# Kernel tuning notes

Hardware: AMD Instinct MI355X
Metric: run time of the kernel (lower is better)

## Reference

```python
import jax, jax.numpy as jnp
import numpy as np

N = 50000          # nodes
E = 1_600_000      # edges (avg degree 32)
D = 128            # input_dim
H = 128            # hidden_dim
EPS = 1e-5


def setup_inputs() -> dict:
    key = jax.random.key(0)
    ks = jax.random.split(key, 8)
    x = jax.random.normal(ks[0], (N, D), jnp.float32)
    edge_index = jax.random.randint(ks[1], (2, E), 0, N)
    message = jax.random.normal(ks[2], (E, H), jnp.float32)

    def lin(k, fin, fout):
        return jax.random.normal(k, (fin, fout), jnp.float32) / np.sqrt(fin).astype(np.float32)

    return {
        "x": x,
        "message": message,
        "W1": lin(ks[3], D + 2 * H, H), "b1": jnp.zeros((H,), jnp.float32),
        "g1": jnp.ones((H,), jnp.float32), "be1": jnp.zeros((H,), jnp.float32),
        "W2": lin(ks[4], H, H), "b2": jnp.zeros((H,), jnp.float32),
        "g2": jnp.ones((H,), jnp.float32), "be2": jnp.zeros((H,), jnp.float32),
        "Wa": lin(ks[5], H, 1), "ba": jnp.zeros((1,), jnp.float32),
        "edge_index": edge_index,
    }


def _batchnorm(h, g, b):
    # training-mode BatchNorm1d: biased batch stats over the node dim
    mu = h.mean(axis=0)
    var = h.var(axis=0)
    return (h - mu) * jax.lax.rsqrt(var + EPS) * g + b


def reference(x, message, W1, b1, g1, be1, W2, b2, g2, be2, Wa, ba, edge_index):
    row, col = edge_index[0], edge_index[1]
    n = x.shape[0]

    def smax(idx):
        m = jax.ops.segment_max(message, idx, num_segments=n)  # [N, H]
        # torch_scatter scatter(reduce='max') leaves empty slots at 0
        return jnp.where(jnp.isfinite(m), m, jnp.zeros_like(m))

    fwd = smax(col)
    bwd = smax(row)
    out = jnp.concatenate([x, fwd, bwd], axis=1)  # [N, D+2H]

    h = jax.nn.relu(_batchnorm(out @ W1 + b1, g1, be1))  # dropout = identity (eval)
    h = jax.nn.relu(_batchnorm(h @ W2 + b2, g2, be2))
    att = jax.nn.sigmoid(h @ Wa + ba).reshape(-1)        # [N]
    return h, att
```

## Files before the change

kernel.cpp:

```cpp
#include <hip/hip_runtime.h>
#include <math.h>

#define N_NODES 50000
#define N_EDGES 1600000
#define DIM 128
#define EPS 1e-5f
#define CAP 96

typedef short bf16x8 __attribute__((ext_vector_type(8)));
typedef float f32x4 __attribute__((ext_vector_type(4)));
typedef int i32x4 __attribute__((ext_vector_type(4)));
typedef unsigned short ushort_t;

__device__ __forceinline__ f32x4 v4max(f32x4 a, f32x4 b) {
    f32x4 r;
    r[0] = fmaxf(a[0], b[0]); r[1] = fmaxf(a[1], b[1]);
    r[2] = fmaxf(a[2], b[2]); r[3] = fmaxf(a[3], b[3]);
    return r;
}

__device__ __forceinline__ ushort_t f2bf(float f) {
    unsigned int u = __float_as_uint(f);
    return (ushort_t)((u + 0x7FFFu + ((u >> 16) & 1u)) >> 16);
}
__device__ __forceinline__ float bf2f(ushort_t u) {
    return __uint_as_float(((unsigned int)u) << 16);
}

__global__ __launch_bounds__(256) void k_prep(const float* __restrict__ W1, const float* __restrict__ W2,
                                              ushort_t* __restrict__ W1t, ushort_t* __restrict__ W2t) {
    int gid = blockIdx.x * 256 + threadIdx.x;
    if (gid < 128 * 384) {
        int j = gid / 384, k = gid % 384;
        W1t[gid] = f2bf(W1[k * 128 + j]);
    } else {
        int g2 = gid - 128 * 384;
        if (g2 < 128 * 128) {
            int j = g2 / 128, k = g2 % 128;
            W2t[g2] = f2bf(W2[k * 128 + j]);
        }
    }
}

__global__ __launch_bounds__(256) void k_bucket(const int* __restrict__ ei, int* __restrict__ cnt,
                                                int* __restrict__ slots) {
    int t = blockIdx.x * 256 + threadIdx.x;
    if (t >= N_EDGES / 4) return;
    int4 r4 = reinterpret_cast<const int4*>(ei)[t];
    int4 c4 = reinterpret_cast<const int4*>(ei + N_EDGES)[t];
    int e = t * 4;
    slots[c4.x * CAP + atomicAdd(&cnt[c4.x], 1)] = e + 0;
    slots[c4.y * CAP + atomicAdd(&cnt[c4.y], 1)] = e + 1;
    slots[c4.z * CAP + atomicAdd(&cnt[c4.z], 1)] = e + 2;
    slots[c4.w * CAP + atomicAdd(&cnt[c4.w], 1)] = e + 3;
    slots[(N_NODES + r4.x) * CAP + atomicAdd(&cnt[N_NODES + r4.x], 1)] = e + 0;
    slots[(N_NODES + r4.y) * CAP + atomicAdd(&cnt[N_NODES + r4.y], 1)] = e + 1;
    slots[(N_NODES + r4.z) * CAP + atomicAdd(&cnt[N_NODES + r4.z], 1)] = e + 2;
    slots[(N_NODES + r4.w) * CAP + atomicAdd(&cnt[N_NODES + r4.w], 1)] = e + 3;
}

__global__ __launch_bounds__(256) void k_gather(const f32x4* __restrict__ msgv,
                                                const int* __restrict__ slots,
                                                const int* __restrict__ cnt,
                                                ushort_t* __restrict__ fwd,
                                                ushort_t* __restrict__ bwd) {
    const int wid = blockIdx.x * 4 + (threadIdx.x >> 6);
    const int dir = (wid >= N_NODES);
    const int n = dir ? wid - N_NODES : wid;
    const int lane = threadIdx.x & 63;
    const int q = lane & 31;
    const int h = lane >> 5;
    const int c = cnt[dir * N_NODES + n];
    const int* el = slots + (size_t)(dir * N_NODES + n) * CAP;

    f32x4 acc0 = {-INFINITY, -INFINITY, -INFINITY, -INFINITY};
    f32x4 acc1 = acc0;
    const int nfull = c >> 2;
    int g = h;
    for (; g + 2 < nfull; g += 4) {
        i32x4 ea = *reinterpret_cast<const i32x4*>(el + g * 4);
        i32x4 eb = *reinterpret_cast<const i32x4*>(el + (g + 2) * 4);
        f32x4 m0 = __builtin_nontemporal_load(&msgv[(size_t)ea[0] * 32 + q]);
        f32x4 m1 = __builtin_nontemporal_load(&msgv[(size_t)ea[1] * 32 + q]);
        f32x4 m2 = __builtin_nontemporal_load(&msgv[(size_t)ea[2] * 32 + q]);
        f32x4 m3 = __builtin_nontemporal_load(&msgv[(size_t)ea[3] * 32 + q]);
        f32x4 m4 = __builtin_nontemporal_load(&msgv[(size_t)eb[0] * 32 + q]);
        f32x4 m5 = __builtin_nontemporal_load(&msgv[(size_t)eb[1] * 32 + q]);
        f32x4 m6 = __builtin_nontemporal_load(&msgv[(size_t)eb[2] * 32 + q]);
        f32x4 m7 = __builtin_nontemporal_load(&msgv[(size_t)eb[3] * 32 + q]);
        acc0 = v4max(acc0, v4max(v4max(m0, m1), v4max(m2, m3)));
        acc1 = v4max(acc1, v4max(v4max(m4, m5), v4max(m6, m7)));
    }
    for (; g < nfull; g += 2) {
        i32x4 e4 = *reinterpret_cast<const i32x4*>(el + g * 4);
        f32x4 m0 = __builtin_nontemporal_load(&msgv[(size_t)e4[0] * 32 + q]);
        f32x4 m1 = __builtin_nontemporal_load(&msgv[(size_t)e4[1] * 32 + q]);
        f32x4 m2 = __builtin_nontemporal_load(&msgv[(size_t)e4[2] * 32 + q]);
        f32x4 m3 = __builtin_nontemporal_load(&msgv[(size_t)e4[3] * 32 + q]);
        acc0 = v4max(acc0, v4max(v4max(m0, m1), v4max(m2, m3)));
    }
    if (h == (nfull & 1)) {
        for (int p = nfull * 4; p < c; ++p) {
            acc1 = v4max(acc1, __builtin_nontemporal_load(&msgv[(size_t)el[p] * 32 + q]));
        }
    }
    f32x4 acc = v4max(acc0, acc1);
    acc[0] = fmaxf(acc[0], __shfl_xor(acc[0], 32));
    acc[1] = fmaxf(acc[1], __shfl_xor(acc[1], 32));
    acc[2] = fmaxf(acc[2], __shfl_xor(acc[2], 32));
    acc[3] = fmaxf(acc[3], __shfl_xor(acc[3], 32));

    if (h == 0) {
        if (c == 0) { acc[0] = 0.f; acc[1] = 0.f; acc[2] = 0.f; acc[3] = 0.f; }
        ushort_t pk[4] = {f2bf(acc[0]), f2bf(acc[1]), f2bf(acc[2]), f2bf(acc[3])};
        ushort_t* dst = (dir ? bwd : fwd) + n * DIM + q * 4;
        *reinterpret_cast<uint2*>(dst) = *reinterpret_cast<const uint2*>(pk);
    }
}


__global__ __launch_bounds__(256) void k_gemm1(const float* __restrict__ x,
                                               const ushort_t* __restrict__ fwd,
                                               const ushort_t* __restrict__ bwd,
                                               const ushort_t* __restrict__ W1t,
                                               const float* __restrict__ b1,
                                               ushort_t* __restrict__ h1b,
                                               float* __restrict__ stats) {
    __shared__ uint4 rowsA4[512];
    __shared__ uint4 Wt4[1024];
    __shared__ float bias[128];
    __shared__ float s_sum[128], s_sq[128];
    char* rowsA = (char*)rowsA4;
    char* Wt = (char*)Wt4;

    const int tid = threadIdx.x;
    const int wid = tid >> 6;
    const int lane = tid & 63;
    const int ln15 = lane & 15;
    const int kb16 = (lane >> 4) * 16;
    const int n0 = blockIdx.x * 64;
    const int rA = wid * 16 + ln15;
    const int rsw = (rA & 7) << 4;

    if (tid < 128) { bias[tid] = b1[tid]; s_sum[tid] = 0.0f; s_sq[tid] = 0.0f; }

    f32x4 acc[8];
#pragma unroll
    for (int i = 0; i < 8; ++i) acc[i] = (f32x4){0.0f, 0.0f, 0.0f, 0.0f};

    for (int c = 0; c < 6; ++c) {
        const int koff = (c & 1) * 64;
        __syncthreads();
        if (c < 2) {
#pragma unroll
            for (int i = 0; i < 2; ++i) {
                int g = tid + i * 256;
                int r = g >> 3, k8 = g & 7;
                int n = n0 + r;
                f32x4 v0 = {0.f, 0.f, 0.f, 0.f}, v1 = v0;
                if (n < N_NODES) {
                    const f32x4* p = reinterpret_cast<const f32x4*>(x + n * DIM + koff + k8 * 8);
                    v0 = __builtin_nontemporal_load(p);
                    v1 = __builtin_nontemporal_load(p + 1);
                }
                ushort_t pk[8] = {f2bf(v0[0]), f2bf(v0[1]), f2bf(v0[2]), f2bf(v0[3]),
                                  f2bf(v1[0]), f2bf(v1[1]), f2bf(v1[2]), f2bf(v1[3])};
                *(uint4*)(rowsA + ((r * 128 + k8 * 16) ^ ((r & 7) << 4))) = *(const uint4*)pk;
            }
        } else {
            const ushort_t* src16 = (c < 4) ? fwd : bwd;
#pragma unroll
            for (int i = 0; i < 2; ++i) {
                int g = tid + i * 256;
                int r = g >> 3, k8 = g & 7;
                int n = n0 + r;
                uint4 v = make_uint4(0u, 0u, 0u, 0u);
                if (n < N_NODES) v = *reinterpret_cast<const uint4*>(src16 + n * DIM + koff + k8 * 8);
                *(uint4*)(rowsA + ((r * 128 + k8 * 16) ^ ((r & 7) << 4))) = v;
            }
        }
#pragma unroll
        for (int i = 0; i < 4; ++i) {
            int g = tid + i * 256;
            int j = g >> 3, k8 = g & 7;
            uint4 w = *reinterpret_cast<const uint4*>(W1t + j * 384 + c * 64 + k8 * 8);
            *(uint4*)(Wt + ((j * 128 + k8 * 16) ^ ((j & 7) << 4))) = w;
        }
        __syncthreads();
#pragma unroll
        for (int ks = 0; ks < 2; ++ks) {
            bf16x8 a = *(bf16x8*)(rowsA + ((rA * 128 + ks * 64 + kb16) ^ rsw));
#pragma unroll
            for (int ct = 0; ct < 8; ++ct) {
                int j = ct * 16 + ln15;
                bf16x8 b = *(bf16x8*)(Wt + ((j * 128 + ks * 64 + kb16) ^ ((j & 7) << 4)));
                acc[ct] = __builtin_amdgcn_mfma_f32_16x16x32_bf16(a, b, acc[ct], 0, 0, 0);
            }
        }
    }
    __syncthreads();
    const int jcol = ln15;
#pragma unroll
    for (int ct = 0; ct < 8; ++ct) {
        int j = ct * 16 + jcol;
        float bj = bias[j];
        float s = 0.0f, q = 0.0f;
#pragma unroll
        for (int r = 0; r < 4; ++r) {
            int n = n0 + wid * 16 + (lane >> 4) * 4 + r;
            if (n < N_NODES) {
                float v = acc[ct][r] + bj;
                h1b[n * DIM + j] = f2bf(v);
                s += v; q += v * v;
            }
        }
        s += __shfl_xor(s, 16); s += __shfl_xor(s, 32);
        q += __shfl_xor(q, 16); q += __shfl_xor(q, 32);
        if ((lane >> 4) == 0) { atomicAdd(&s_sum[j], s); atomicAdd(&s_sq[j], q); }
    }
    __syncthreads();
    if (tid < 128) {
        atomicAdd(&stats[tid], s_sum[tid]);
        atomicAdd(&stats[128 + tid], s_sq[tid]);
    }
}

__global__ __launch_bounds__(256) void k_gemm2(const ushort_t* __restrict__ h1b,
                                               const ushort_t* __restrict__ W2t,
                                               const float* __restrict__ b2,
                                               const float* __restrict__ g1,
                                               const float* __restrict__ be1,
                                               ushort_t* __restrict__ h2b,
                                               float* __restrict__ stats) {
    __shared__ uint4 rowsA4[512];
    __shared__ uint4 Wt4[1024];
    __shared__ float bias[128];
    __shared__ float ssc[128], ssh[128];
    __shared__ float s_sum[128], s_sq[128];
    char* rowsA = (char*)rowsA4;
    char* Wt = (char*)Wt4;

    const int tid = threadIdx.x;
    const int wid = tid >> 6;
    const int lane = tid & 63;
    const int ln15 = lane & 15;
    const int kb16 = (lane >> 4) * 16;
    const int n0 = blockIdx.x * 64;
    const int rA = wid * 16 + ln15;
    const int rsw = (rA & 7) << 4;

    if (tid < 128) {
        float mu = stats[tid] * (1.0f / N_NODES);
        float var = stats[128 + tid] * (1.0f / N_NODES) - mu * mu;
        float sc = rsqrtf(var + EPS) * g1[tid];
        ssc[tid] = sc;
        ssh[tid] = be1[tid] - mu * sc;
        bias[tid] = b2[tid];
        s_sum[tid] = 0.0f; s_sq[tid] = 0.0f;
    }

    f32x4 acc[8];
#pragma unroll
    for (int i = 0; i < 8; ++i) acc[i] = (f32x4){0.0f, 0.0f, 0.0f, 0.0f};

    for (int c = 0; c < 2; ++c) {
        const int koff = c * 64;
        __syncthreads();
#pragma unroll
        for (int i = 0; i < 2; ++i) {
            int g = tid + i * 256;
            int r = g >> 3, k8 = g & 7;
            int n = n0 + r;
            ushort_t pk[8] = {0, 0, 0, 0, 0, 0, 0, 0};
            if (n < N_NODES) {
                uint4 raw = *reinterpret_cast<const uint4*>(h1b + n * DIM + koff + k8 * 8);
                const ushort_t* rp = (const ushort_t*)&raw;
#pragma unroll
                for (int t = 0; t < 8; ++t) {
                    int kk = koff + k8 * 8 + t;
                    float v = fmaxf(bf2f(rp[t]) * ssc[kk] + ssh[kk], 0.0f);
                    pk[t] = f2bf(v);
                }
            }
            *(uint4*)(rowsA + ((r * 128 + k8 * 16) ^ ((r & 7) << 4))) = *(const uint4*)pk;
        }
#pragma unroll
        for (int i = 0; i < 4; ++i) {
            int g = tid + i * 256;
            int j = g >> 3, k8 = g & 7;
            uint4 w = *reinterpret_cast<const uint4*>(W2t + j * 128 + c * 64 + k8 * 8);
            *(uint4*)(Wt + ((j * 128 + k8 * 16) ^ ((j & 7) << 4))) = w;
        }
        __syncthreads();
#pragma unroll
        for (int ks = 0; ks < 2; ++ks) {
            bf16x8 a = *(bf16x8*)(rowsA + ((rA * 128 + ks * 64 + kb16) ^ rsw));
#pragma unroll
            for (int ct = 0; ct < 8; ++ct) {
                int j = ct * 16 + ln15;
                bf16x8 b = *(bf16x8*)(Wt + ((j * 128 + ks * 64 + kb16) ^ ((j & 7) << 4)));
                acc[ct] = __builtin_amdgcn_mfma_f32_16x16x32_bf16(a, b, acc[ct], 0, 0, 0);
            }
        }
    }
    __syncthreads();
    const int jcol = ln15;
#pragma unroll
    for (int ct = 0; ct < 8; ++ct) {
        int j = ct * 16 + jcol;
        float bj = bias[j];
        float s = 0.0f, q = 0.0f;
#pragma unroll
        for (int r = 0; r < 4; ++r) {
            int n = n0 + wid * 16 + (lane >> 4) * 4 + r;
            if (n < N_NODES) {
                float v = acc[ct][r] + bj;
                h2b[n * DIM + j] = f2bf(v);
                s += v; q += v * v;
            }
        }
        s += __shfl_xor(s, 16); s += __shfl_xor(s, 32);
        q += __shfl_xor(q, 16); q += __shfl_xor(q, 32);
        if ((lane >> 4) == 0) { atomicAdd(&s_sum[j], s); atomicAdd(&s_sq[j], q); }
    }
    __syncthreads();
    if (tid < 128) {
        atomicAdd(&stats[256 + tid], s_sum[tid]);
        atomicAdd(&stats[384 + tid], s_sq[tid]);
    }
}

__global__ __launch_bounds__(256) void k_final(const ushort_t* __restrict__ h2b,
                                               const float* __restrict__ stats,
                                               const float* __restrict__ g2,
                                               const float* __restrict__ be2,
                                               const float* __restrict__ Wa,
                                               const float* __restrict__ ba,
                                               float* __restrict__ out) {
    const int lane = threadIdx.x & 63;
    const int wv = threadIdx.x >> 6;
    const int n = blockIdx.x * 4 + wv;
    if (n >= N_NODES) return;
    const int j0 = lane, j1 = lane + 64;

    float mu0 = stats[256 + j0] * (1.0f / N_NODES);
    float var0 = stats[384 + j0] * (1.0f / N_NODES) - mu0 * mu0;
    float sc0 = rsqrtf(var0 + EPS) * g2[j0];
    float sh0 = be2[j0] - mu0 * sc0;
    float mu1 = stats[256 + j1] * (1.0f / N_NODES);
    float var1 = stats[384 + j1] * (1.0f / N_NODES) - mu1 * mu1;
    float sc1 = rsqrtf(var1 + EPS) * g2[j1];
    float sh1 = be2[j1] - mu1 * sc1;

    float v0 = fmaxf(bf2f(h2b[n * DIM + j0]) * sc0 + sh0, 0.0f);
    float v1 = fmaxf(bf2f(h2b[n * DIM + j1]) * sc1 + sh1, 0.0f);
    out[n * DIM + j0] = v0;
    out[n * DIM + j1] = v1;

    float p = v0 * Wa[j0] + v1 * Wa[j1];
#pragma unroll
    for (int off = 32; off > 0; off >>= 1) p += __shfl_down(p, off);
    if (lane == 0) out[N_NODES * DIM + n] = 1.0f / (1.0f + expf(-(p + ba[0])));
}

extern "C" void kernel_launch(void* const* d_in, const int* in_sizes, int n_in,
                              void* d_out, int out_size, void* d_ws, size_t ws_size,
                              hipStream_t stream) {
    const float* x   = (const float*)d_in[0];
    const float* msg = (const float*)d_in[1];
    const float* W1  = (const float*)d_in[2];
    const float* b1  = (const float*)d_in[3];
    const float* g1  = (const float*)d_in[4];
    const float* be1 = (const float*)d_in[5];
    const float* W2  = (const float*)d_in[6];
    const float* b2  = (const float*)d_in[7];
    const float* g2  = (const float*)d_in[8];
    const float* be2 = (const float*)d_in[9];
    const float* Wa  = (const float*)d_in[10];
    const float* ba  = (const float*)d_in[11];
    const int*   ei  = (const int*)d_in[12];

    float*    stats = (float*)d_ws;
    ushort_t* fwdb  = (ushort_t*)(stats + 512);
    ushort_t* bwdb  = fwdb + N_NODES * DIM;
    int*      cnt   = (int*)(bwdb + N_NODES * DIM);
    int*      slots = cnt + 2 * N_NODES;
    ushort_t* W1t   = (ushort_t*)(slots + 2 * N_NODES * CAP);
    ushort_t* W2t   = W1t + 128 * 384;

    ushort_t* h1b = (ushort_t*)d_out;
    ushort_t* h2b = fwdb;
    float*    out = (float*)d_out;

    (void)hipMemsetAsync(stats, 0, 512 * sizeof(float), stream);
    (void)hipMemsetAsync(cnt, 0, 2 * N_NODES * sizeof(int), stream);
    k_prep<<<(128 * 384 + 128 * 128 + 255) / 256, 256, 0, stream>>>(W1, W2, W1t, W2t);
    k_bucket<<<(N_EDGES / 4 + 255) / 256, 256, 0, stream>>>(ei, cnt, slots);
    k_gather<<<(2 * N_NODES) / 4, 256, 0, stream>>>((const f32x4*)msg, slots, cnt, fwdb, bwdb);
    k_gemm1<<<(N_NODES + 63) / 64, 256, 0, stream>>>(x, fwdb, bwdb, W1t, b1, h1b, stats);
    k_gemm2<<<(N_NODES + 63) / 64, 256, 0, stream>>>(h1b, W2t, b2, g1, be1, h2b, stats);
    k_final<<<(N_NODES + 3) / 4, 256, 0, stream>>>(h2b, stats, g2, be2, Wa, ba, out);
}
```

Measured before the change: 621.2 us.

## Pre-convert messages to bf16 in bucketing kernel and gather bf16 rows

New measurement: 690.0 us. 11.1% more time.

```diff
diff --git a/kernel.cpp b/kernel.cpp
--- a/kernel.cpp
+++ b/kernel.cpp
@@ -10,21 +10,20 @@
 typedef short bf16x8 __attribute__((ext_vector_type(8)));
 typedef float f32x4 __attribute__((ext_vector_type(4)));
 typedef int i32x4 __attribute__((ext_vector_type(4)));
+typedef unsigned int u32x2 __attribute__((ext_vector_type(2)));
 typedef unsigned short ushort_t;
 
-__device__ __forceinline__ f32x4 v4max(f32x4 a, f32x4 b) {
-    f32x4 r;
-    r[0] = fmaxf(a[0], b[0]); r[1] = fmaxf(a[1], b[1]);
-    r[2] = fmaxf(a[2], b[2]); r[3] = fmaxf(a[3], b[3]);
-    return r;
-}
-
-__device__ __forceinline__ ushort_t f2bf(float f) {
+__device__ __forceinline__ unsigned int f2bf(float f) {
     unsigned int u = __float_as_uint(f);
-    return (ushort_t)((u + 0x7FFFu + ((u >> 16) & 1u)) >> 16);
+    return (u + 0x7FFFu + ((u >> 16) & 1u)) >> 16;
 }
 __device__ __forceinline__ float bf2f(ushort_t u) {
     return __uint_as_float(((unsigned int)u) << 16);
+}
+
+__device__ __forceinline__ void wmax(unsigned int w, float& lo, float& hi) {
+    lo = fmaxf(lo, __uint_as_float(w << 16));
+    hi = fmaxf(hi, __uint_as_float(w & 0xFFFF0000u));
 }
 
 __global__ __launch_bounds__(256) void k_prep(const float* __restrict__ W1, const float* __restrict__ W2,
@@ -32,34 +31,46 @@
     int gid = blockIdx.x * 256 + threadIdx.x;
     if (gid < 128 * 384) {
         int j = gid / 384, k = gid % 384;
-        W1t[gid] = f2bf(W1[k * 128 + j]);
+        W1t[gid] = (ushort_t)f2bf(W1[k * 128 + j]);
     } else {
         int g2 = gid - 128 * 384;
         if (g2 < 128 * 128) {
             int j = g2 / 128, k = g2 % 128;
-            W2t[g2] = f2bf(W2[k * 128 + j]);
-        }
-    }
-}
-
-__global__ __launch_bounds__(256) void k_bucket(const int* __restrict__ ei, int* __restrict__ cnt,
-                                                int* __restrict__ slots) {
+            W2t[g2] = (ushort_t)f2bf(W2[k * 128 + j]);
+        }
+    }
+}
+
+__global__ __launch_bounds__(256) void k_bucketconv(const int* __restrict__ ei, int* __restrict__ cnt,
+                                                    int* __restrict__ slots,
+                                                    const f32x4* __restrict__ msg,
+                                                    u32x2* __restrict__ msgb) {
     int t = blockIdx.x * 256 + threadIdx.x;
-    if (t >= N_EDGES / 4) return;
-    int4 r4 = reinterpret_cast<const int4*>(ei)[t];
-    int4 c4 = reinterpret_cast<const int4*>(ei + N_EDGES)[t];
-    int e = t * 4;
-    slots[c4.x * CAP + atomicAdd(&cnt[c4.x], 1)] = e + 0;
-    slots[c4.y * CAP + atomicAdd(&cnt[c4.y], 1)] = e + 1;
-    slots[c4.z * CAP + atomicAdd(&cnt[c4.z], 1)] = e + 2;
-    slots[c4.w * CAP + atomicAdd(&cnt[c4.w], 1)] = e + 3;
-    slots[(N_NODES + r4.x) * CAP + atomicAdd(&cnt[N_NODES + r4.x], 1)] = e + 0;
-    slots[(N_NODES + r4.y) * CAP + atomicAdd(&cnt[N_NODES + r4.y], 1)] = e + 1;
-    slots[(N_NODES + r4.z) * CAP + atomicAdd(&cnt[N_NODES + r4.z], 1)] = e + 2;
-    slots[(N_NODES + r4.w) * CAP + atomicAdd(&cnt[N_NODES + r4.w], 1)] = e + 3;
-}
-
-__global__ __launch_bounds__(256) void k_gather(const f32x4* __restrict__ msgv,
+    if (t < N_EDGES / 4) {
+        int4 r4 = reinterpret_cast<const int4*>(ei)[t];
+        int4 c4 = reinterpret_cast<const int4*>(ei + N_EDGES)[t];
+        int e = t * 4;
+        slots[c4.x * CAP + atomicAdd(&cnt[c4.x], 1)] = e + 0;
+        slots[c4.y * CAP + atomicAdd(&cnt[c4.y], 1)] = e + 1;
+        slots[c4.z * CAP + atomicAdd(&cnt[c4.z], 1)] = e + 2;
+        slots[c4.w * CAP + atomicAdd(&cnt[c4.w], 1)] = e + 3;
+        slots[(N_NODES + r4.x) * CAP + atomicAdd(&cnt[N_NODES + r4.x], 1)] = e + 0;
+        slots[(N_NODES + r4.y) * CAP + atomicAdd(&cnt[N_NODES + r4.y], 1)] = e + 1;
+        slots[(N_NODES + r4.z) * CAP + atomicAdd(&cnt[N_NODES + r4.z], 1)] = e + 2;
+        slots[(N_NODES + r4.w) * CAP + atomicAdd(&cnt[N_NODES + r4.w], 1)] = e + 3;
+    }
+    const size_t total = (size_t)N_EDGES * 32;
+    const size_t stride = (size_t)gridDim.x * 256;
+    for (size_t v = t; v < total; v += stride) {
+        f32x4 m = __builtin_nontemporal_load(&msg[v]);
+        u32x2 o;
+        o[0] = f2bf(m[0]) | (f2bf(m[1]) << 16);
+        o[1] = f2bf(m[2]) | (f2bf(m[3]) << 16);
+        msgb[v] = o;
+    }
+}
+
+__global__ __launch_bounds__(256) void k_gather(const u32x2* __restrict__ msgb,
                                                 const int* __restrict__ slots,
                                                 const int* __restrict__ cnt,
                                                 ushort_t* __restrict__ fwd,
@@ -73,48 +84,62 @@
     const int c = cnt[dir * N_NODES + n];
     const int* el = slots + (size_t)(dir * N_NODES + n) * CAP;
 
-    f32x4 acc0 = {-INFINITY, -INFINITY, -INFINITY, -INFINITY};
-    f32x4 acc1 = acc0;
+    float l0a = -INFINITY, h0a = -INFINITY, l1a = -INFINITY, h1a = -INFINITY;
+    float l0b = -INFINITY, h0b = -INFINITY, l1b = -INFINITY, h1b = -INFINITY;
     const int nfull = c >> 2;
     int g = h;
     for (; g + 2 < nfull; g += 4) {
         i32x4 ea = *reinterpret_cast<const i32x4*>(el + g * 4);
         i32x4 eb = *reinterpret_cast<const i32x4*>(el + (g + 2) * 4);
-        f32x4 m0 = __builtin_nontemporal_load(&msgv[(size_t)ea[0] * 32 + q]);
-        f32x4 m1 = __builtin_nontemporal_load(&msgv[(size_t)ea[1] * 32 + q]);
-        f32x4 m2 = __builtin_nontemporal_load(&msgv[(size_t)ea[2] * 32 + q]);
-        f32x4 m3 = __builtin_nontemporal_load(&msgv[(size_t)ea[3] * 32 + q]);
-        f32x4 m4 = __builtin_nontemporal_load(&msgv[(size_t)eb[0] * 32 + q]);
-        f32x4 m5 = __builtin_nontemporal_load(&msgv[(size_t)eb[1] * 32 + q]);
-        f32x4 m6 = __builtin_nontemporal_load(&msgv[(size_t)eb[2] * 32 + q]);
-        f32x4 m7 = __builtin_nontemporal_load(&msgv[(size_t)eb[3] * 32 + q]);
-        acc0 = v4max(acc0, v4max(v4max(m0, m1), v4max(m2, m3)));
-        acc1 = v4max(acc1, v4max(v4max(m4, m5), v4max(m6, m7)));
+        u32x2 m0 = msgb[(size_t)ea[0] * 32 + q];
+        u32x2 m1 = msgb[(size_t)ea[1] * 32 + q];
+        u32x2 m2 = msgb[(size_t)ea[2] * 32 + q];
+        u32x2 m3 = msgb[(size_t)ea[3] * 32 + q];
+        u32x2 m4 = msgb[(size_t)eb[0] * 32 + q];
+        u32x2 m5 = msgb[(size_t)eb[1] * 32 + q];
+        u32x2 m6 = msgb[(size_t)eb[2] * 32 + q];
+        u32x2 m7 = msgb[(size_t)eb[3] * 32 + q];
+        wmax(m0[0], l0a, h0a); wmax(m0[1], l1a, h1a);
+        wmax(m1[0], l0a, h0a); wmax(m1[1], l1a, h1a);
+        wmax(m2[0], l0a, h0a); wmax(m2[1], l1a, h1a);
+        wmax(m3[0], l0a, h0a); wmax(m3[1], l1a, h1a);
+        wmax(m4[0], l0b, h0b); wmax(m4[1], l1b, h1b);
+        wmax(m5[0], l0b, h0b); wmax(m5[1], l1b, h1b);
+        wmax(m6[0], l0b, h0b); wmax(m6[1], l1b, h1b);
+        wmax(m7[0], l0b, h0b); wmax(m7[1], l1b, h1b);
     }
     for (; g < nfull; g += 2) {
         i32x4 e4 = *reinterpret_cast<const i32x4*>(el + g * 4);
-        f32x4 m0 = __builtin_nontemporal_load(&msgv[(size_t)e4[0] * 32 + q]);
-        f32x4 m1 = __builtin_nontemporal_load(&msgv[(size_t)e4[1] * 32 + q]);
-        f32x4 m2 = __builtin_nontemporal_load(&msgv[(size_t)e4[2] * 32 + q]);
-        f32x4 m3 = __builtin_nontemporal_load(&msgv[(size_t)e4[3] * 32 + q]);
-        acc0 = v4max(acc0, v4max(v4max(m0, m1), v4max(m2, m3)));
+        u32x2 m0 = msgb[(size_t)e4[0] * 32 + q];
+        u32x2 m1 = msgb[(size_t)e4[1] * 32 + q];
+        u32x2 m2 = msgb[(size_t)e4[2] * 32 + q];
+        u32x2 m3 = msgb[(size_t)e4[3] * 32 + q];
+        wmax(m0[0], l0a, h0a); wmax(m0[1], l1a, h1a);
+        wmax(m1[0], l0a, h0a); wmax(m1[1], l1a, h1a);
+        wmax(m2[0], l0a, h0a); wmax(m2[1], l1a, h1a);
+        wmax(m3[0], l0a, h0a); wmax(m3[1], l1a, h1a);
     }
     if (h == (nfull & 1)) {
         for (int p = nfull * 4; p < c; ++p) {
-            acc1 = v4max(acc1, __builtin_nontemporal_load(&msgv[(size_t)el[p] * 32 + q]));
-        }
-    }
-    f32x4 acc = v4max(acc0, acc1);
-    acc[0] = fmaxf(acc[0], __shfl_xor(acc[0], 32));
-    acc[1] = fmaxf(acc[1], __shfl_xor(acc[1], 32));
-    acc[2] = fmaxf(acc[2], __shfl_xor(acc[2], 32));
-    acc[3] = fmaxf(acc[3], __shfl_xor(acc[3], 32));
+            u32x2 m = msgb[(size_t)el[p] * 32 + q];
+            wmax(m[0], l0b, h0b); wmax(m[1], l1b, h1b);
+        }
+    }
+    float l0 = fmaxf(l0a, l0b), h0 = fmaxf(h0a, h0b);
+    float l1 = fmaxf(l1a, l1b), h1 = fmaxf(h1a, h1b);
+    l0 = fmaxf(l0, __shfl_xor(l0, 32));
+    h0 = fmaxf(h0, __shfl_xor(h0, 32));
+    l1 = fmaxf(l1, __shfl_xor(l1, 32));
+    h1 = fmaxf(h1, __shfl_xor(h1, 32));
 
     if (h == 0) {
-        if (c == 0) { acc[0] = 0.f; acc[1] = 0.f; acc[2] = 0.f; acc[3] = 0.f; }
-        ushort_t pk[4] = {f2bf(acc[0]), f2bf(acc[1]), f2bf(acc[2]), f2bf(acc[3])};
-        ushort_t* dst = (dir ? bwd : fwd) + n * DIM + q * 4;
-        *reinterpret_cast<uint2*>(dst) = *reinterpret_cast<const uint2*>(pk);
+        u32x2 o;
+        if (c == 0) { o[0] = 0u; o[1] = 0u; }
+        else {
+            o[0] = (__float_as_uint(l0) >> 16) | (__float_as_uint(h0) & 0xFFFF0000u);
+            o[1] = (__float_as_uint(l1) >> 16) | (__float_as_uint(h1) & 0xFFFF0000u);
+        }
+        *reinterpret_cast<u32x2*>((dir ? bwd : fwd) + n * DIM + q * 4) = o;
     }
 }
 
@@ -163,8 +188,10 @@
                     v0 = __builtin_nontemporal_load(p);
                     v1 = __builtin_nontemporal_load(p + 1);
                 }
-                ushort_t pk[8] = {f2bf(v0[0]), f2bf(v0[1]), f2bf(v0[2]), f2bf(v0[3]),
-                                  f2bf(v1[0]), f2bf(v1[1]), f2bf(v1[2]), f2bf(v1[3])};
+                ushort_t pk[8] = {(ushort_t)f2bf(v0[0]), (ushort_t)f2bf(v0[1]),
+                                  (ushort_t)f2bf(v0[2]), (ushort_t)f2bf(v0[3]),
+                                  (ushort_t)f2bf(v1[0]), (ushort_t)f2bf(v1[1]),
+                                  (ushort_t)f2bf(v1[2]), (ushort_t)f2bf(v1[3])};
                 *(uint4*)(rowsA + ((r * 128 + k8 * 16) ^ ((r & 7) << 4))) = *(const uint4*)pk;
             }
         } else {
@@ -210,7 +237,7 @@
             int n = n0 + wid * 16 + (lane >> 4) * 4 + r;
             if (n < N_NODES) {
                 float v = acc[ct][r] + bj;
-                h1b[n * DIM + j] = f2bf(v);
+                h1b[n * DIM + j] = (ushort_t)f2bf(v);
                 s += v; q += v * v;
             }
         }
@@ -279,7 +306,7 @@
                 for (int t = 0; t < 8; ++t) {
                     int kk = koff + k8 * 8 + t;
                     float v = fmaxf(bf2f(rp[t]) * ssc[kk] + ssh[kk], 0.0f);
-                    pk[t] = f2bf(v);
+                    pk[t] = (ushort_t)f2bf(v);
                 }
             }
             *(uint4*)(rowsA + ((r * 128 + k8 * 16) ^ ((r & 7) << 4))) = *(const uint4*)pk;
@@ -315,7 +342,7 @@
             int n = n0 + wid * 16 + (lane >> 4) * 4 + r;
             if (n < N_NODES) {
                 float v = acc[ct][r] + bj;
-                h2b[n * DIM + j] = f2bf(v);
+                h2b[n * DIM + j] = (ushort_t)f2bf(v);
                 s += v; q += v * v;
             }
         }
@@ -387,6 +414,7 @@
     int*      slots = cnt + 2 * N_NODES;
     ushort_t* W1t   = (ushort_t*)(slots + 2 * N_NODES * CAP);
     ushort_t* W2t   = W1t + 128 * 384;
+    u32x2*    msgb  = (u32x2*)(W2t + 128 * 128 + 128);
 
     ushort_t* h1b = (ushort_t*)d_out;
     ushort_t* h2b = fwdb;
@@ -395,8 +423,8 @@
     (void)hipMemsetAsync(stats, 0, 512 * sizeof(float), stream);
     (void)hipMemsetAsync(cnt, 0, 2 * N_NODES * sizeof(int), stream);
     k_prep<<<(128 * 384 + 128 * 128 + 255) / 256, 256, 0, stream>>>(W1, W2, W1t, W2t);
-    k_bucket<<<(N_EDGES / 4 + 255) / 256, 256, 0, stream>>>(ei, cnt, slots);
-    k_gather<<<(2 * N_NODES) / 4, 256, 0, stream>>>((const f32x4*)msg, slots, cnt, fwdb, bwdb);
+    k_bucketconv<<<2048, 256, 0, stream>>>(ei, cnt, slots, (const f32x4*)msg, msgb);
+    k_gather<<<(2 * N_NODES) / 4, 256, 0, stream>>>(msgb, slots, cnt, fwdb, bwdb);
     k_gemm1<<<(N_NODES + 63) / 64, 256, 0, stream>>>(x, fwdb, bwdb, W1t, b1, h1b, stats);
     k_gemm2<<<(N_NODES + 63) / 64, 256, 0, stream>>>(h1b, W2t, b2, g1, be1, h2b, stats);
     k_final<<<(N_NODES + 3) / 4, 256, 0, stream>>>(h2b, stats, g2, be2, Wa, ba, out);
```
